# Kernel optimization log

Measured on AMD Instinct MI355X. Metric: run time of the kernel, lower is better.

The kernel has to match this reference:

```python
import jax, jax.numpy as jnp
import numpy as np

DIM = 2048
DIM_HEAD = 128
HEADS = 16
FF_MULT = 4
EPS = 1e-05
ATTN_INNER = DIM_HEAD * HEADS          # 2048
FF_INNER = DIM * FF_MULT               # 8192
FUSED_DIMS = (ATTN_INNER, DIM_HEAD, DIM_HEAD, FF_INNER, FF_INNER)
SPLITS = np.cumsum(FUSED_DIMS[:-1]).tolist()
RMS_SCALE = DIM ** 0.5
Q_SCALE = DIM_HEAD ** (-0.5)


def setup_inputs() -> dict:
    key = jax.random.key(0)
    k1, k2, k3, k4, k5 = jax.random.split(key, 5)
    B, S = 2, 2048
    x = jax.random.normal(k1, (B, S, DIM), dtype=jnp.float32)
    attn_bias = jax.random.normal(k2, (HEADS, S, S), dtype=jnp.float32)
    # learned params (scaled for numerical sanity; math identical to module)
    gamma = jnp.ones((DIM,), dtype=jnp.float32)
    wi = jax.random.normal(k3, (DIM, sum(FUSED_DIMS)), dtype=jnp.float32) * 0.02
    attn_wo = jax.random.normal(k4, (ATTN_INNER, DIM), dtype=jnp.float32) * 0.02
    ff_wo = jax.random.normal(k5, (FF_INNER, DIM), dtype=jnp.float32) * 0.02
    return {"x": x, "attn_bias": attn_bias, "gamma": gamma,
            "wi": wi, "attn_wo": attn_wo, "ff_wo": ff_wo}


def reference(x, attn_bias, gamma, wi, attn_wo, ff_wo):
    B, S, _ = x.shape
    # RMSNorm
    inv_norm = jax.lax.rsqrt(jnp.sum(jnp.square(x), axis=-1, keepdims=True) + EPS)
    xn = inv_norm * x * gamma * RMS_SCALE
    # fused projection
    proj = xn @ wi  # [B, S, sum(fused_dims)]
    q, k, v, ff, ff_gate = jnp.split(proj, SPLITS, axis=-1)
    # q: [B, S, H*Dh] -> [B, H, S, Dh]; k, v stay single-head [B, S, Dh] (MQA)
    q = q.reshape(B, S, HEADS, DIM_HEAD).transpose(0, 2, 1, 3) * Q_SCALE
    sim = jnp.einsum('bhid,bjd->bhij', q, k) + attn_bias  # [B, H, S, S]
    attn = jax.nn.softmax(sim, axis=-1)
    out = jnp.einsum('bhij,bjd->bhid', attn, v)  # [B, H, S, Dh]
    out = out.transpose(0, 2, 1, 3).reshape(B, S, ATTN_INNER)
    attn_out = out @ attn_wo
    ff_out = (ff * jax.nn.swish(ff_gate)) @ ff_wo
    return attn_out + ff_out
```

## Files before the change

kernel.cpp:

```cpp
#include <hip/hip_runtime.h>
#include <cstdint>

typedef unsigned short u16;
typedef short bf16x8 __attribute__((ext_vector_type(8)));
typedef float f32x4 __attribute__((ext_vector_type(4)));

#define PLD 18688
#define ALD 10240
#define LOG2E 1.4426950408889634f
#define QSCALE 0.08838834764831845f
#define RMS_SCALE 45.25483399593904f

__device__ __forceinline__ u16 f2bf(float f) {
  union { float f; unsigned int u; } v; v.f = f;
  unsigned int u = v.u;
  return (u16)((u + 0x7fffu + ((u >> 16) & 1u)) >> 16);
}
__device__ __forceinline__ float bf2f(u16 h) {
  union { unsigned int u; float f; } v; v.u = ((unsigned int)h) << 16;
  return v.f;
}

__device__ __forceinline__ void gload_lds16(const void* g, void* l) {
  __builtin_amdgcn_global_load_lds((__attribute__((address_space(1))) void*)(g),
                                   (__attribute__((address_space(3))) void*)(l),
                                   16, 0, 0);
}

__global__ __launch_bounds__(256) void rmsnorm_kernel(const float* __restrict__ x,
                                                      const float* __restrict__ gamma,
                                                      u16* __restrict__ xn) {
  const int row = blockIdx.x;
  const int tid = threadIdx.x;
  const float4* xr = (const float4*)(x + (size_t)row * 2048);
  float4 v0 = xr[tid], v1 = xr[tid + 256];
  float s = v0.x*v0.x + v0.y*v0.y + v0.z*v0.z + v0.w*v0.w
          + v1.x*v1.x + v1.y*v1.y + v1.z*v1.z + v1.w*v1.w;
  for (int m = 1; m < 64; m <<= 1) s += __shfl_xor(s, m, 64);
  __shared__ float red[4];
  if ((tid & 63) == 0) red[tid >> 6] = s;
  __syncthreads();
  float tot = red[0] + red[1] + red[2] + red[3];
  float inv = rsqrtf(tot + 1e-5f) * RMS_SCALE;
  const float4* gp = (const float4*)gamma;
  float4 g0 = gp[tid], g1 = gp[tid + 256];
  u16* xo = xn + (size_t)row * 2048;
  union { u16 h[4]; uint2 u; } o0, o1;
  o0.h[0] = f2bf(v0.x*inv*g0.x); o0.h[1] = f2bf(v0.y*inv*g0.y);
  o0.h[2] = f2bf(v0.z*inv*g0.z); o0.h[3] = f2bf(v0.w*inv*g0.w);
  o1.h[0] = f2bf(v1.x*inv*g1.x); o1.h[1] = f2bf(v1.y*inv*g1.y);
  o1.h[2] = f2bf(v1.z*inv*g1.z); o1.h[3] = f2bf(v1.w*inv*g1.w);
  *(uint2*)(xo + tid*4) = o0.u;
  *(uint2*)(xo + (tid+256)*4) = o1.u;
}

__global__ __launch_bounds__(256) void tconv(const float* __restrict__ src,
                                             u16* __restrict__ dst,
                                             int K, int N, int dstride, int doff) {
  __shared__ u16 t[32][33];
  const int tx = threadIdx.x & 31, ty = threadIdx.x >> 5;
  const int n0 = blockIdx.x * 32, k0 = blockIdx.y * 32;
  #pragma unroll
  for (int yy = 0; yy < 4; yy++) {
    int r = ty + yy*8;
    t[r][tx] = f2bf(src[(size_t)(k0 + r) * N + n0 + tx]);
  }
  __syncthreads();
  #pragma unroll
  for (int yy = 0; yy < 4; yy++) {
    int r = ty + yy*8;
    dst[(size_t)(n0 + r) * dstride + doff + k0 + tx] = t[tx][r];
  }
}

template <int OUT_BF16, int GC>
__global__ __launch_bounds__(256) void gemm_bt(const u16* __restrict__ A,
                                               const u16* __restrict__ Bt,
                                               void* __restrict__ Cv,
                                               int M, int N, int K) {
  __shared__ alignas(16) u16 sA[128*32];
  __shared__ alignas(16) u16 sB[128*32];
  const int numRow = M >> 7;
  const int per = GC * numRow;
  const int pid = blockIdx.x;
  const int g = pid / per, inner = pid % per;
  const int colT = g * GC + inner / numRow;
  const int rowT = inner % numRow;
  const int row0 = rowT * 128, col0 = colT * 128;

  const int tid = threadIdx.x;
  const int w = tid >> 6, lane = tid & 63, quad = lane >> 4, l16 = lane & 15;
  const int wr = (w >> 1) * 64, wc = (w & 1) * 64;
  const f32x4 zero = {0.f, 0.f, 0.f, 0.f};
  f32x4 acc[4][4];
  #pragma unroll
  for (int mi = 0; mi < 4; mi++)
    #pragma unroll
    for (int ni = 0; ni < 4; ni++) acc[mi][ni] = zero;

  for (int k0 = 0; k0 < K; k0 += 32) {
    __syncthreads();
    #pragma unroll
    for (int i = 0; i < 2; i++) {
      const int segbase = (i*4 + w) * 64;
      const int seg = segbase + lane;
      const int r = seg >> 2, c = (seg & 3) * 8;
      gload_lds16(A  + (size_t)(row0 + r) * K + k0 + c, sA + segbase * 8);
      gload_lds16(Bt + (size_t)(col0 + r) * K + k0 + c, sB + segbase * 8);
    }
    __syncthreads();
    bf16x8 af[4], bfr[4];
    #pragma unroll
    for (int mi = 0; mi < 4; mi++)
      af[mi] = *(const bf16x8*)&sA[(wr + mi*16 + l16)*32 + quad*8];
    #pragma unroll
    for (int ni = 0; ni < 4; ni++)
      bfr[ni] = *(const bf16x8*)&sB[(wc + ni*16 + l16)*32 + quad*8];
    #pragma unroll
    for (int mi = 0; mi < 4; mi++)
      #pragma unroll
      for (int ni = 0; ni < 4; ni++)
        acc[mi][ni] = __builtin_amdgcn_mfma_f32_16x16x32_bf16(af[mi], bfr[ni], acc[mi][ni], 0, 0, 0);
  }

  #pragma unroll
  for (int mi = 0; mi < 4; mi++) {
    const int rb = row0 + wr + mi*16 + quad*4;
    #pragma unroll
    for (int ni = 0; ni < 4; ni++) {
      const int cb = col0 + wc + ni*16 + l16;
      #pragma unroll
      for (int r = 0; r < 4; r++) {
        if (OUT_BF16) ((u16*)Cv)[(size_t)(rb + r) * N + cb] = f2bf(acc[mi][ni][r]);
        else          ((float*)Cv)[(size_t)(rb + r) * N + cb] = acc[mi][ni][r];
      }
    }
  }
}

__global__ __launch_bounds__(256) void ffh_kernel(const u16* __restrict__ proj,
                                                  u16* __restrict__ amat) {
  const int idx = blockIdx.x * 256 + threadIdx.x;
  const int row = idx >> 11;
  const int c = (idx & 2047) * 4;
  const u16* pr = proj + (size_t)row * PLD;
  uint2 fu = *(const uint2*)(pr + 2304 + c);
  uint2 gu = *(const uint2*)(pr + 10496 + c);
  u16 f[4] = {(u16)(fu.x & 0xffffu), (u16)(fu.x >> 16), (u16)(fu.y & 0xffffu), (u16)(fu.y >> 16)};
  u16 g[4] = {(u16)(gu.x & 0xffffu), (u16)(gu.x >> 16), (u16)(gu.y & 0xffffu), (u16)(gu.y >> 16)};
  union { u16 h[4]; uint2 u; } o;
  #pragma unroll
  for (int e = 0; e < 4; e++) {
    float gg = bf2f(g[e]);
    float sw = gg / (1.f + __expf(-gg));
    o.h[e] = f2bf(bf2f(f[e]) * sw);
  }
  *(uint2*)(amat + (size_t)row * ALD + 2048 + c) = o.u;
}

__global__ __launch_bounds__(256) void attn_kernel(const u16* __restrict__ proj,
                                                   const float* __restrict__ bias,
                                                   u16* __restrict__ amat) {
  const int it = blockIdx.x, h = blockIdx.y, b = blockIdx.z;
  const int tid = threadIdx.x;
  const int w = tid >> 6, lane = tid & 63, quad = lane >> 4, l16 = lane & 15;
  const int i0 = it * 64;
  __shared__ alignas(16) u16 kt[64*128];
  __shared__ alignas(16) u16 vt[128*72];
  __shared__ alignas(16) u16 pl[4][16*72];

  bf16x8 qf[4];
  {
    const u16* qp = proj + (size_t)(b*2048 + i0 + w*16 + l16) * PLD + h*128 + quad*8;
    #pragma unroll
    for (int kst = 0; kst < 4; kst++) qf[kst] = *(const bf16x8*)(qp + kst*32);
  }
  const f32x4 zero = {0.f, 0.f, 0.f, 0.f};
  f32x4 of[8];
  #pragma unroll
  for (int nd = 0; nd < 8; nd++) of[nd] = zero;
  float m_r[4] = {-1e30f, -1e30f, -1e30f, -1e30f};
  float l_r[4] = {0.f, 0.f, 0.f, 0.f};

  for (int j0 = 0; j0 < 2048; j0 += 64) {
    __syncthreads();
    #pragma unroll
    for (int i = 0; i < 4; i++) {
      const int segbase = (i*4 + w) * 64;
      const int seg = segbase + lane;
      const int r = seg >> 4, c = (seg & 15) * 8;
      gload_lds16(proj + (size_t)(b*2048 + j0 + r) * PLD + 2048 + c, kt + segbase*8);
    }
    #pragma unroll
    for (int e = 0; e < 16; e++) {
      const int flat = e*256 + tid;
      const int j = flat >> 6, d2 = (flat & 63) * 2;
      const unsigned int pv = *(const unsigned int*)(proj + (size_t)(b*2048 + j0 + j)*PLD + 2176 + d2);
      vt[d2*72 + j]     = (u16)(pv & 0xffffu);
      vt[(d2+1)*72 + j] = (u16)(pv >> 16);
    }
    __syncthreads();

    f32x4 sf[4];
    #pragma unroll
    for (int nj = 0; nj < 4; nj++) sf[nj] = zero;
    #pragma unroll
    for (int kst = 0; kst < 4; kst++)
      #pragma unroll
      for (int nj = 0; nj < 4; nj++) {
        bf16x8 bfr = *(const bf16x8*)&kt[(nj*16 + l16)*128 + kst*32 + quad*8];
        sf[nj] = __builtin_amdgcn_mfma_f32_16x16x32_bf16(qf[kst], bfr, sf[nj], 0, 0, 0);
      }

    const float* bp = bias + ((size_t)h*2048 + (i0 + w*16 + quad*4)) * 2048 + j0 + l16;
    float s[4][4];
    #pragma unroll
    for (int nj = 0; nj < 4; nj++)
      #pragma unroll
      for (int r = 0; r < 4; r++)
        s[nj][r] = sf[nj][r] * QSCALE + bp[(size_t)r*2048 + nj*16];

    float p[4][4]; float alpha[4];
    #pragma unroll
    for (int r = 0; r < 4; r++) {
      float rm = fmaxf(fmaxf(s[0][r], s[1][r]), fmaxf(s[2][r], s[3][r]));
      rm = fmaxf(rm, __shfl_xor(rm, 1, 64));
      rm = fmaxf(rm, __shfl_xor(rm, 2, 64));
      rm = fmaxf(rm, __shfl_xor(rm, 4, 64));
      rm = fmaxf(rm, __shfl_xor(rm, 8, 64));
      const float mn = fmaxf(m_r[r], rm);
      alpha[r] = exp2f((m_r[r] - mn) * LOG2E);
      m_r[r] = mn;
      float rs = 0.f;
      #pragma unroll
      for (int nj = 0; nj < 4; nj++) { p[nj][r] = exp2f((s[nj][r] - mn) * LOG2E); rs += p[nj][r]; }
      rs += __shfl_xor(rs, 1, 64);
      rs += __shfl_xor(rs, 2, 64);
      rs += __shfl_xor(rs, 4, 64);
      rs += __shfl_xor(rs, 8, 64);
      l_r[r] = l_r[r] * alpha[r] + rs;
    }
    #pragma unroll
    for (int nd = 0; nd < 8; nd++)
      #pragma unroll
      for (int r = 0; r < 4; r++) of[nd][r] *= alpha[r];

    #pragma unroll
    for (int nj = 0; nj < 4; nj++)
      #pragma unroll
      for (int r = 0; r < 4; r++)
        pl[w][(quad*4 + r)*72 + nj*16 + l16] = f2bf(p[nj][r]);
    __syncthreads();

    #pragma unroll
    for (int k2 = 0; k2 < 2; k2++) {
      bf16x8 af = *(const bf16x8*)&pl[w][l16*72 + k2*32 + quad*8];
      #pragma unroll
      for (int nd = 0; nd < 8; nd++) {
        bf16x8 bfr = *(const bf16x8*)&vt[(nd*16 + l16)*72 + k2*32 + quad*8];
        of[nd] = __builtin_amdgcn_mfma_f32_16x16x32_bf16(af, bfr, of[nd], 0, 0, 0);
      }
    }
  }

  const int token = b*2048 + i0 + w*16 + quad*4;
  #pragma unroll
  for (int r = 0; r < 4; r++) {
    const float invl = 1.f / l_r[r];
    u16* op = amat + (size_t)(token + r) * ALD + h*128 + l16;
    #pragma unroll
    for (int nd = 0; nd < 8; nd++) op[nd*16] = f2bf(of[nd][r] * invl);
  }
}

extern "C" void kernel_launch(void* const* d_in, const int* in_sizes, int n_in,
                              void* d_out, int out_size, void* d_ws, size_t ws_size,
                              hipStream_t stream) {
  const float* x       = (const float*)d_in[0];
  const float* bias    = (const float*)d_in[1];
  const float* gamma   = (const float*)d_in[2];
  const float* wi      = (const float*)d_in[3];
  const float* attn_wo = (const float*)d_in[4];
  const float* ff_wo   = (const float*)d_in[5];
  float* out = (float*)d_out;

  char* ws = (char*)d_ws;
  u16* xn   = (u16*)(ws);
  u16* wiT  = (u16*)(ws + 16777216);
  u16* amat = (u16*)(ws);
  u16* woT  = (u16*)(ws + 93323264);
  u16* proj = (u16*)(ws + 135266304);

  rmsnorm_kernel<<<4096, 256, 0, stream>>>(x, gamma, xn);
  tconv<<<dim3(18688/32, 2048/32), 256, 0, stream>>>(wi, wiT, 2048, 18688, 2048, 0);
  tconv<<<dim3(2048/32, 2048/32), 256, 0, stream>>>(attn_wo, woT, 2048, 2048, 10240, 0);
  tconv<<<dim3(2048/32, 8192/32), 256, 0, stream>>>(ff_wo, woT, 8192, 2048, 10240, 2048);
  gemm_bt<1, 8><<<146*32, 256, 0, stream>>>(xn, wiT, proj, 4096, 18688, 2048);
  ffh_kernel<<<32768, 256, 0, stream>>>(proj, amat);
  attn_kernel<<<dim3(32, 16, 2), 256, 0, stream>>>(proj, bias, amat);
  gemm_bt<0, 16><<<16*32, 256, 0, stream>>>(amat, woT, out, 4096, 2048, 10240);
}
```

Baseline: 1.648 ms.

## Add 256x256-tile 8-wave GEMM with interleaved LDS pipeline for fused projection

Adds a new bf16 GEMM kernel that uses 256x256 output tiles with 512 threads. It double-buffers K-slices in LDS through direct global-to-LDS loads interleaved with MFMA phases, raises wave priority around the MFMA blocks, and remaps block IDs so tiles are grouped per XCD. The input projection GEMM (4096x18688x2048) now uses this kernel in place of the 128-tile gemm_bt, aiming for more data reuse per tile and better overlap of loads with math. The larger tile uses 128KB of LDS and many accumulator registers, which limits occupancy. It also relies on N being divisible by 256, which holds for 18688 (73 tiles).

```diff
diff --git a/kernel.cpp b/kernel.cpp
--- a/kernel.cpp
+++ b/kernel.cpp
@@ -138,6 +138,147 @@
   }
 }
 
+#define BAR() do { asm volatile("" ::: "memory"); __builtin_amdgcn_s_barrier(); asm volatile("" ::: "memory"); } while (0)
+#define WAITV(N) asm volatile("s_waitcnt vmcnt(" #N ")" ::: "memory")
+
+template <int OUT_BF16>
+__global__ __launch_bounds__(512, 2) void gemm256(const u16* __restrict__ A,
+                                                  const u16* __restrict__ Bt,
+                                                  void* __restrict__ Cv,
+                                                  int M, int N, int K) {
+  __shared__ alignas(16) u16 lds[65536];
+  u16* const sB = lds + 32768;
+
+  const int numRow = M >> 8;
+  int pid = blockIdx.x;
+  {
+    const int nwg = gridDim.x;
+    const int q = nwg >> 3, r = nwg & 7;
+    const int xcd = pid & 7, lid = pid >> 3;
+    pid = (xcd < r ? xcd * (q + 1) : r * (q + 1) + (xcd - r) * q) + lid;
+  }
+  const int colT = pid / numRow, rowT = pid % numRow;
+  const int row0 = rowT << 8, col0 = colT << 8;
+
+  const int tid = threadIdx.x;
+  const int w = tid >> 6, lane = tid & 63, quad = lane >> 4, l16 = lane & 15;
+  const int wr = w >> 2, wc = w & 3;
+
+  const u16* aG  = A  + (size_t)(row0 + w * 16 + l16) * K + quad * 8;
+  const u16* aG2 = aG + (size_t)128 * K;
+  const u16* bG  = Bt + (size_t)(col0 + w * 16 + l16) * K + quad * 8;
+  const u16* bG2 = bG + (size_t)128 * K;
+
+  #define STAGE_A(bb, ks, kt) do { \
+    gload_lds16(aG  + (kt) + (ks) * 32, lds + (bb) * 16384 + (ks) * 8192 + w * 512); \
+    gload_lds16(aG2 + (kt) + (ks) * 32, lds + (bb) * 16384 + (ks) * 8192 + (8 + w) * 512); \
+  } while (0)
+  #define STAGE_B(bb, ks, kt) do { \
+    gload_lds16(bG  + (kt) + (ks) * 32, sB + (bb) * 16384 + (ks) * 8192 + w * 512); \
+    gload_lds16(bG2 + (kt) + (ks) * 32, sB + (bb) * 16384 + (ks) * 8192 + (8 + w) * 512); \
+  } while (0)
+
+  const f32x4 zero = {0.f, 0.f, 0.f, 0.f};
+  f32x4 acc[8][4];
+  #pragma unroll
+  for (int mi = 0; mi < 8; mi++)
+    #pragma unroll
+    for (int ni = 0; ni < 4; ni++) acc[mi][ni] = zero;
+
+  const int nt = K >> 6;
+  STAGE_A(0, 0, 0);  STAGE_B(0, 0, 0);
+  STAGE_A(0, 1, 0);  STAGE_B(0, 1, 0);
+  STAGE_A(1, 0, 64); STAGE_B(1, 0, 64);
+  WAITV(8);
+  BAR();
+
+  const int aBase = wr * 8 * 512 + lane * 8;
+  const int bBase = wc * 4 * 512 + lane * 8;
+
+  for (int t = 0; t < nt; ++t) {
+    const int bb = t & 1, nb = bb ^ 1;
+    const int kt1 = (t + 1) << 6, kt2 = (t + 2) << 6;
+    bf16x8 af[8], bf0, bf1;
+
+    #pragma unroll
+    for (int mi = 0; mi < 8; mi++)
+      af[mi] = *(const bf16x8*)(lds + bb * 16384 + aBase + mi * 512);
+    bf0 = *(const bf16x8*)(sB + bb * 16384 + bBase);
+    bf1 = *(const bf16x8*)(sB + bb * 16384 + bBase + 512);
+    if (t + 1 < nt) STAGE_A(nb, 1, kt1);
+    BAR();
+    __builtin_amdgcn_s_setprio(1);
+    #pragma unroll
+    for (int mi = 0; mi < 8; mi++) {
+      acc[mi][0] = __builtin_amdgcn_mfma_f32_16x16x32_bf16(af[mi], bf0, acc[mi][0], 0, 0, 0);
+      acc[mi][1] = __builtin_amdgcn_mfma_f32_16x16x32_bf16(af[mi], bf1, acc[mi][1], 0, 0, 0);
+    }
+    __builtin_amdgcn_s_setprio(0);
+    BAR();
+
+    bf0 = *(const bf16x8*)(sB + bb * 16384 + bBase + 1024);
+    bf1 = *(const bf16x8*)(sB + bb * 16384 + bBase + 1536);
+    if (t + 1 < nt) STAGE_B(nb, 1, kt1);
+    BAR();
+    __builtin_amdgcn_s_setprio(1);
+    #pragma unroll
+    for (int mi = 0; mi < 8; mi++) {
+      acc[mi][2] = __builtin_amdgcn_mfma_f32_16x16x32_bf16(af[mi], bf0, acc[mi][2], 0, 0, 0);
+      acc[mi][3] = __builtin_amdgcn_mfma_f32_16x16x32_bf16(af[mi], bf1, acc[mi][3], 0, 0, 0);
+    }
+    __builtin_amdgcn_s_setprio(0);
+    if (t + 1 < nt) { WAITV(8); } else { WAITV(0); }
+    BAR();
+
+    #pragma unroll
+    for (int mi = 0; mi < 8; mi++)
+      af[mi] = *(const bf16x8*)(lds + bb * 16384 + 8192 + aBase + mi * 512);
+    bf0 = *(const bf16x8*)(sB + bb * 16384 + 8192 + bBase);
+    bf1 = *(const bf16x8*)(sB + bb * 16384 + 8192 + bBase + 512);
+    if (t + 2 < nt) STAGE_A(bb, 0, kt2);
+    BAR();
+    __builtin_amdgcn_s_setprio(1);
+    #pragma unroll
+    for (int mi = 0; mi < 8; mi++) {
+      acc[mi][0] = __builtin_amdgcn_mfma_f32_16x16x32_bf16(af[mi], bf0, acc[mi][0], 0, 0, 0);
+      acc[mi][1] = __builtin_amdgcn_mfma_f32_16x16x32_bf16(af[mi], bf1, acc[mi][1], 0, 0, 0);
+    }
+    __builtin_amdgcn_s_setprio(0);
+    BAR();
+
+    bf0 = *(const bf16x8*)(sB + bb * 16384 + 8192 + bBase + 1024);
+    bf1 = *(const bf16x8*)(sB + bb * 16384 + 8192 + bBase + 1536);
+    if (t + 2 < nt) STAGE_B(bb, 0, kt2);
+    BAR();
+    __builtin_amdgcn_s_setprio(1);
+    #pragma unroll
+    for (int mi = 0; mi < 8; mi++) {
+      acc[mi][2] = __builtin_amdgcn_mfma_f32_16x16x32_bf16(af[mi], bf0, acc[mi][2], 0, 0, 0);
+      acc[mi][3] = __builtin_amdgcn_mfma_f32_16x16x32_bf16(af[mi], bf1, acc[mi][3], 0, 0, 0);
+    }
+    __builtin_amdgcn_s_setprio(0);
+    if (t + 2 < nt)      { WAITV(8); }
+    else if (t + 1 < nt) { WAITV(4); }
+    BAR();
+  }
+  #undef STAGE_A
+  #undef STAGE_B
+
+  #pragma unroll
+  for (int mi = 0; mi < 8; mi++) {
+    const int rb = row0 + wr*128 + mi*16 + quad*4;
+    #pragma unroll
+    for (int ni = 0; ni < 4; ni++) {
+      const int cb = col0 + wc*64 + ni*16 + l16;
+      #pragma unroll
+      for (int r = 0; r < 4; r++) {
+        if (OUT_BF16) ((u16*)Cv)[(size_t)(rb + r) * N + cb] = f2bf(acc[mi][ni][r]);
+        else          ((float*)Cv)[(size_t)(rb + r) * N + cb] = acc[mi][ni][r];
+      }
+    }
+  }
+}
+
 __global__ __launch_bounds__(256) void ffh_kernel(const u16* __restrict__ proj,
                                                   u16* __restrict__ amat) {
   const int idx = blockIdx.x * 256 + threadIdx.x;
@@ -295,7 +436,7 @@
   tconv<<<dim3(18688/32, 2048/32), 256, 0, stream>>>(wi, wiT, 2048, 18688, 2048, 0);
   tconv<<<dim3(2048/32, 2048/32), 256, 0, stream>>>(attn_wo, woT, 2048, 2048, 10240, 0);
   tconv<<<dim3(2048/32, 8192/32), 256, 0, stream>>>(ff_wo, woT, 8192, 2048, 10240, 2048);
-  gemm_bt<1, 8><<<146*32, 256, 0, stream>>>(xn, wiT, proj, 4096, 18688, 2048);
+  gemm256<1><<<73*16, 512, 0, stream>>>(xn, wiT, proj, 4096, 18688, 2048);
   ffh_kernel<<<32768, 256, 0, stream>>>(proj, amat);
   attn_kernel<<<dim3(32, 16, 2), 256, 0, stream>>>(proj, bias, amat);
   gemm_bt<0, 16><<<16*32, 256, 0, stream>>>(amat, woT, out, 4096, 2048, 10240);
```

New measurement: 1.575 ms. 4.4% less time.
